# Kernel optimization log

Hardware: AMD Instinct MI355X
Metric: run time of the kernel (lower is better)

## Reference

```python
import jax, jax.numpy as jnp
import numpy as np


def setup_inputs() -> dict:
    key = jax.random.key(0)
    k1, k2 = jax.random.split(key)
    H, W, C = 1024, 2048, 32
    img = jax.random.normal(k1, (1, C, H, W), dtype=jnp.float32)
    flow = jax.random.normal(k2, (1, 2, H, W), dtype=jnp.float32)
    return {"img": img, "flow": flow, "H": H, "W": W}


def reference(img, flow, H, W):
    # img: [1, C, H, W], flow: [1, 2, H, W]
    C = img.shape[1]
    u = flow[:, 0, :, :]  # [1, H, W]
    v = flow[:, 1, :, :]
    grid_x = jnp.arange(W, dtype=jnp.float32)[None, None, :]  # [1,1,W]
    grid_y = jnp.arange(H, dtype=jnp.float32)[None, :, None]  # [1,H,1]
    x = grid_x + u  # [1, H, W]
    y = grid_y + v
    # normalize to [-1, 1] then back (faithful to original two-step mapping)
    x = 2.0 * (x / (W - 1) - 0.5)
    y = 2.0 * (y / (H - 1) - 0.5)
    x = (x + 1.0) * 0.5 * (W - 1)
    y = (y + 1.0) * 0.5 * (H - 1)

    x0 = jnp.floor(x)
    x1 = x0 + 1.0
    y0 = jnp.floor(y)
    y1 = y0 + 1.0
    x0c = jnp.clip(x0, 0, W - 1).astype(jnp.int32)
    x1c = jnp.clip(x1, 0, W - 1).astype(jnp.int32)
    y0c = jnp.clip(y0, 0, H - 1).astype(jnp.int32)
    y1c = jnp.clip(y1, 0, H - 1).astype(jnp.int32)

    # bilinear weights from UNCLAMPED coords (as in the original)
    wa = (x1 - x) * (y1 - y)
    wb = (x1 - x) * (y - y0)
    wc = (x - x0) * (y1 - y)
    wd = (x - x0) * (y - y0)

    img_flat = jnp.transpose(img[0], (1, 2, 0)).reshape(H * W, C)  # [H*W, C]

    def gather_pixel(ix, iy):
        idx = (iy * W + ix).reshape(-1)  # [H*W]
        return jnp.take(img_flat, idx, axis=0)  # [H*W, C]

    Ia = gather_pixel(x0c, y0c)
    Ib = gather_pixel(x0c, y1c)
    Ic = gather_pixel(x1c, y0c)
    Id = gather_pixel(x1c, y1c)

    out = (Ia * wa.reshape(-1, 1) + Ib * wb.reshape(-1, 1)
           + Ic * wc.reshape(-1, 1) + Id * wd.reshape(-1, 1))  # [H*W, C]
    out = out.reshape(1, H, W, C)
    return jnp.transpose(out, (0, 3, 1, 2))  # [1, C, H, W]
```

## Files before the change

kernel.cpp:

```cpp
#include <hip/hip_runtime.h>


#define TSX 64
#define TSY 32
#define RAD 4
#define LW  (TSX + 2*RAD)
#define LH  (TSY + 2*RAD)
#define GPR (LW/4)
#define PLANE (LW*LH)
#define NV  (LH*GPR)
#define CGB 2
#define NSTG (CGB*NV)
#define NTHREADS 1024
#define SOFF (NSTG - NTHREADS)

static_assert(NSTG >= NTHREADS && NSTG <= 2*NTHREADS, "2 slots per thread");

#define GLOAD_LDS16(g, l)                                                  \
    __builtin_amdgcn_global_load_lds(                                      \
        (const __attribute__((address_space(1))) void*)(g),                \
        (__attribute__((address_space(3))) void*)(l), 16, 0, 0)

__global__ __launch_bounds__(NTHREADS, 8) void warp_pipe3(
    const float* __restrict__ img,
    const float* __restrict__ flow,
    const int* __restrict__ Hp,
    const int* __restrict__ Wp,
    float* __restrict__ out,
    int HW, int C)
{
    __shared__ __align__(16) float lds[2 * CGB * PLANE];

    const int W = *Wp;
    const int H = *Hp;
    const int tilesX = (W + TSX - 1) / TSX;
    const int tilesY = (H + TSY - 1) / TSY;
    const int ntiles = tilesX * tilesY;
    const int bid = blockIdx.x;
    if (bid >= ntiles) return;

    const int q = ntiles >> 3, r = ntiles & 7;
    const int xcd = bid & 7, sub = bid >> 3;
    const int t = (xcd < r ? xcd*(q+1) : r*(q+1) + (xcd-r)*q) + sub;

    const int tileY = t / tilesX;
    const int tileX = t - tileY * tilesX;
    const int gx0 = tileX * TSX - RAD;
    const int gy0 = tileY * TSY - RAD;

    const int tid = threadIdx.x;
    const int lx  = tid & 63;
    const int rw  = (tid >> 6) * 2;
    const int gx  = tileX * TSX + lx;

    const float Wm1 = (float)(W - 1);
    const float Hm1 = (float)(H - 1);

    float wtl[2], wth[2], wbl[2], wbh[2];
    int enc[2], pixk[2] = {0, 0};
    #pragma unroll
    for (int k = 0; k < 2; ++k) {
        const int gy = tileY * TSY + rw + k;
        enc[k] = -2;
        if (gx >= W || gy >= H) continue;
        const int pix = gy * W + gx;
        pixk[k] = pix;
        const float u = flow[pix];
        const float v = flow[HW + pix];

        const float x = (float)gx + u;
        const float y = (float)gy + v;
        const float x0 = floorf(x), x1 = x0 + 1.0f;
        const float y0 = floorf(y), y1 = y0 + 1.0f;

        const int x0c = (int)fminf(fmaxf(x0, 0.0f), Wm1);
        const int x1c = (int)fminf(fmaxf(x1, 0.0f), Wm1);
        const int y0c = (int)fminf(fmaxf(y0, 0.0f), Hm1);
        const int y1c = (int)fminf(fmaxf(y1, 0.0f), Hm1);

        const float wa = (x1 - x) * (y1 - y);
        const float wb = (x1 - x) * (y - y0);
        const float wc = (x - x0) * (y1 - y);
        const float wd = (x - x0) * (y - y0);

        const int pbx = min(x0c, W - 2);
        const int pby = min(y0c, H - 2);

        const float wlt = (x0c == pbx ? wa : 0.f) + (x1c == pbx ? wc : 0.f);
        const float wht = (x0c != pbx ? wa : 0.f) + (x1c != pbx ? wc : 0.f);
        const float wlb = (x0c == pbx ? wb : 0.f) + (x1c == pbx ? wd : 0.f);
        const float whb = (x0c != pbx ? wb : 0.f) + (x1c != pbx ? wd : 0.f);
        const bool t0 = (y0c == pby), t1 = (y1c == pby);
        wtl[k] = (t0 ? wlt : 0.f) + (t1 ? wlb : 0.f);
        wth[k] = (t0 ? wht : 0.f) + (t1 ? whb : 0.f);
        wbl[k] = (t0 ? 0.f : wlt) + (t1 ? 0.f : wlb);
        wbh[k] = (t0 ? 0.f : wht) + (t1 ? 0.f : whb);

        const int lxp = pbx - gx0;
        const int lyb = pby - gy0;
        enc[k] = (lxp >= 0 && lxp <= LW-2 && lyb >= 0 && lyb <= LH-2)
               ? (lyb * LW + lxp) : -1;
    }

    float* optr0 = out + pixk[0];
    float* optr1 = out + pixk[1];

    int spix[2], chrel[2], dst4[2];
    #pragma unroll
    for (int s = 0; s < 2; ++s) {
        const int idx = tid + s * SOFF;
        const int ch  = idx / NV;
        const int rem = idx - ch * NV;
        const int rr  = rem / GPR;
        const int g   = rem - rr * GPR;
        const int yy  = min(max(gy0 + rr, 0), H - 1);
        const int xs  = min(max(gx0 + 4*g, 0), W - 4);
        chrel[s] = ch;
        spix[s]  = yy * W + xs;
        dst4[s]  = idx * 4;
    }

    const int nph = (C + CGB - 1) / CGB;
    const bool fast = ((W & 3) == 0) && ((tileX+1)*TSX <= W)
                   && ((tileY+1)*TSY <= H);

    auto gather2 = [&](const float* cur, int c0) {
        #pragma unroll
        for (int k = 0; k < 2; ++k) {
            const int e = enc[k];
            if (e == -2) continue;
            float* o = (k == 0) ? optr0 : optr1;
            if (__builtin_expect(e >= 0, 1)) {
                const float* b0 = cur + e;
                const float a0 = wtl[k], a1 = wth[k];
                const float a2 = wbl[k], a3 = wbh[k];
                o[0] = a0*b0[0] + a1*b0[1] + a2*b0[LW] + a3*b0[LW+1];
                if (c0 + 1 < C)
                    o[HW] = a0*b0[PLANE]   + a1*b0[PLANE+1]
                          + a2*b0[PLANE+LW] + a3*b0[PLANE+LW+1];
            } else {
                const int pix = pixk[k];
                const int gy  = tileY * TSY + rw + k;
                const float u = flow[pix];
                const float v = flow[HW + pix];
                const float x = (float)gx + u;
                const float y = (float)gy + v;
                const float x0 = floorf(x), y0f = floorf(y);
                const int x0c = (int)fminf(fmaxf(x0, 0.f), Wm1);
                const int x1c = (int)fminf(fmaxf(x0 + 1.f, 0.f), Wm1);
                const int y0c = (int)fminf(fmaxf(y0f, 0.f), Hm1);
                const int y1c = (int)fminf(fmaxf(y0f + 1.f, 0.f), Hm1);
                const float wa = (x0 + 1.f - x) * (y0f + 1.f - y);
                const float wb = (x0 + 1.f - x) * (y - y0f);
                const float wc = (x - x0) * (y0f + 1.f - y);
                const float wd = (x - x0) * (y - y0f);
                for (int c = 0; c < CGB && c0 + c < C; ++c) {
                    const float* ic = img + (size_t)(c0 + c) * HW;
                    o[(size_t)c * HW] =
                          wa * ic[(size_t)y0c*W + x0c] + wb * ic[(size_t)y1c*W + x0c]
                        + wc * ic[(size_t)y0c*W + x1c] + wd * ic[(size_t)y1c*W + x1c];
                }
            }
        }
    };

    if (fast) {
        #pragma unroll
        for (int s = 0; s < 2; ++s) {
            const int chc = min(chrel[s], C - 1);
            GLOAD_LDS16(img + (size_t)chc * HW + spix[s], &lds[dst4[s]]);
        }
        asm volatile("s_waitcnt vmcnt(0)" ::: "memory");
        __builtin_amdgcn_s_barrier();
        __builtin_amdgcn_sched_barrier(0);

        float* cur = &lds[0];
        float* nxt = &lds[CGB * PLANE];

        for (int p = 0; p < nph; ++p) {
            const int c0 = p * CGB;

            if (p + 1 < nph) {
                const int c0n = c0 + CGB;
                #pragma unroll
                for (int s = 0; s < 2; ++s) {
                    const int chc = min(c0n + chrel[s], C - 1);
                    GLOAD_LDS16(img + (size_t)chc * HW + spix[s], nxt + dst4[s]);
                }
            }
            __builtin_amdgcn_sched_barrier(0);

            gather2(cur, c0);

            __builtin_amdgcn_sched_barrier(0);

            if (p + 1 < nph) {
                asm volatile("s_waitcnt vmcnt(4)" ::: "memory");
                __builtin_amdgcn_sched_barrier(0);
                __builtin_amdgcn_s_barrier();
                __builtin_amdgcn_sched_barrier(0);
            }
            float* tmp = cur; cur = nxt; nxt = tmp;
            optr0 += (size_t)CGB * HW;
            optr1 += (size_t)CGB * HW;
        }
    } else {
        for (int p = 0; p < nph; ++p) {
            const int c0 = p * CGB;
            __syncthreads();
            for (int i = tid; i < CGB * PLANE; i += NTHREADS) {
                const int ch  = i / PLANE;
                const int rem = i - ch * PLANE;
                const int rr  = rem / LW;
                const int cc  = rem - rr * LW;
                const int yy  = min(max(gy0 + rr, 0), H - 1);
                const int xx  = min(max(gx0 + cc, 0), W - 1);
                const int chc = min(c0 + ch, C - 1);
                lds[i] = img[(size_t)chc * HW + (size_t)yy * W + xx];
            }
            __syncthreads();
            gather2(&lds[0], c0);
            optr0 += (size_t)CGB * HW;
            optr1 += (size_t)CGB * HW;
        }
    }
}

extern "C" void kernel_launch(void* const* d_in, const int* in_sizes, int n_in,
                              void* d_out, int out_size, void* d_ws, size_t ws_size,
                              hipStream_t stream) {
    const float* img  = (const float*)d_in[0];
    const float* flow = (const float*)d_in[1];
    const int*   Hp   = (const int*)d_in[2];
    const int*   Wp   = (const int*)d_in[3];
    float* out = (float*)d_out;

    const int HW = in_sizes[1] / 2;
    const int C  = in_sizes[0] / HW;

    const int grid = (HW + TSX * TSY - 1) / (TSX * TSY) + 64;
    warp_pipe3<<<grid, NTHREADS, 0, stream>>>(img, flow, Hp, Wp, out, HW, C);
}
```

Baseline: 128.4 us.

## Split block into producer/consumer waves with triple-buffered per-channel LDS staging

Replaces the uniform double-buffered two-channel loop with warp specialization. Half the threads (512) compute bilinear weights for 4 pixels each and gather one channel per phase. The other half issue global-to-LDS async loads two channels ahead into a rotating triple buffer. The goal is to keep loads always in flight, decoupled from the gather work. The cost is one barrier per channel instead of per two channels, fewer threads doing the gather math, and more registers per consumer.

New measurement: 212.1 us. 1.65x slower.

```diff
diff --git a/kernel.cpp b/kernel.cpp
--- a/kernel.cpp
+++ b/kernel.cpp
@@ -9,19 +9,17 @@
 #define GPR (LW/4)
 #define PLANE (LW*LH)
 #define NV  (LH*GPR)
-#define CGB 2
-#define NSTG (CGB*NV)
+#define BUFP 4096
 #define NTHREADS 1024
-#define SOFF (NSTG - NTHREADS)
-
-static_assert(NSTG >= NTHREADS && NSTG <= 2*NTHREADS, "2 slots per thread");
+#define NCONS 512
+#define PXT 4
 
 #define GLOAD_LDS16(g, l)                                                  \
     __builtin_amdgcn_global_load_lds(                                      \
         (const __attribute__((address_space(1))) void*)(g),                \
         (__attribute__((address_space(3))) void*)(l), 16, 0, 0)
 
-__global__ __launch_bounds__(NTHREADS, 8) void warp_pipe3(
+__global__ __launch_bounds__(NTHREADS, 8) void warp_pc(
     const float* __restrict__ img,
     const float* __restrict__ flow,
     const int* __restrict__ Hp,
@@ -29,7 +27,7 @@
     float* __restrict__ out,
     int HW, int C)
 {
-    __shared__ __align__(16) float lds[2 * CGB * PLANE];
+    __shared__ __align__(16) float lds[3 * BUFP];
 
     const int W = *Wp;
     const int H = *Hp;
@@ -49,100 +47,104 @@
     const int gy0 = tileY * TSY - RAD;
 
     const int tid = threadIdx.x;
-    const int lx  = tid & 63;
-    const int rw  = (tid >> 6) * 2;
-    const int gx  = tileX * TSX + lx;
+    const bool consumer = (tid < NCONS);
 
     const float Wm1 = (float)(W - 1);
     const float Hm1 = (float)(H - 1);
 
-    float wtl[2], wth[2], wbl[2], wbh[2];
-    int enc[2], pixk[2] = {0, 0};
-    #pragma unroll
-    for (int k = 0; k < 2; ++k) {
-        const int gy = tileY * TSY + rw + k;
-        enc[k] = -2;
-        if (gx >= W || gy >= H) continue;
-        const int pix = gy * W + gx;
-        pixk[k] = pix;
-        const float u = flow[pix];
-        const float v = flow[HW + pix];
-
-        const float x = (float)gx + u;
-        const float y = (float)gy + v;
-        const float x0 = floorf(x), x1 = x0 + 1.0f;
-        const float y0 = floorf(y), y1 = y0 + 1.0f;
-
-        const int x0c = (int)fminf(fmaxf(x0, 0.0f), Wm1);
-        const int x1c = (int)fminf(fmaxf(x1, 0.0f), Wm1);
-        const int y0c = (int)fminf(fmaxf(y0, 0.0f), Hm1);
-        const int y1c = (int)fminf(fmaxf(y1, 0.0f), Hm1);
-
-        const float wa = (x1 - x) * (y1 - y);
-        const float wb = (x1 - x) * (y - y0);
-        const float wc = (x - x0) * (y1 - y);
-        const float wd = (x - x0) * (y - y0);
-
-        const int pbx = min(x0c, W - 2);
-        const int pby = min(y0c, H - 2);
-
-        const float wlt = (x0c == pbx ? wa : 0.f) + (x1c == pbx ? wc : 0.f);
-        const float wht = (x0c != pbx ? wa : 0.f) + (x1c != pbx ? wc : 0.f);
-        const float wlb = (x0c == pbx ? wb : 0.f) + (x1c == pbx ? wd : 0.f);
-        const float whb = (x0c != pbx ? wb : 0.f) + (x1c != pbx ? wd : 0.f);
-        const bool t0 = (y0c == pby), t1 = (y1c == pby);
-        wtl[k] = (t0 ? wlt : 0.f) + (t1 ? wlb : 0.f);
-        wth[k] = (t0 ? wht : 0.f) + (t1 ? whb : 0.f);
-        wbl[k] = (t0 ? 0.f : wlt) + (t1 ? 0.f : wlb);
-        wbh[k] = (t0 ? 0.f : wht) + (t1 ? 0.f : whb);
-
-        const int lxp = pbx - gx0;
-        const int lyb = pby - gy0;
-        enc[k] = (lxp >= 0 && lxp <= LW-2 && lyb >= 0 && lyb <= LH-2)
-               ? (lyb * LW + lxp) : -1;
-    }
-
-    float* optr0 = out + pixk[0];
-    float* optr1 = out + pixk[1];
-
-    int spix[2], chrel[2], dst4[2];
-    #pragma unroll
-    for (int s = 0; s < 2; ++s) {
-        const int idx = tid + s * SOFF;
-        const int ch  = idx / NV;
-        const int rem = idx - ch * NV;
-        const int rr  = rem / GPR;
-        const int g   = rem - rr * GPR;
-        const int yy  = min(max(gy0 + rr, 0), H - 1);
-        const int xs  = min(max(gx0 + 4*g, 0), W - 4);
-        chrel[s] = ch;
-        spix[s]  = yy * W + xs;
-        dst4[s]  = idx * 4;
-    }
-
-    const int nph = (C + CGB - 1) / CGB;
     const bool fast = ((W & 3) == 0) && ((tileX+1)*TSX <= W)
                    && ((tileY+1)*TSY <= H);
 
-    auto gather2 = [&](const float* cur, int c0) {
+    float a0[PXT], a1[PXT], a2[PXT], a3[PXT];
+    int   enc[PXT];
+    float* optr[PXT];
+    int   pixk[PXT];
+    if (consumer) {
         #pragma unroll
-        for (int k = 0; k < 2; ++k) {
-            const int e = enc[k];
+        for (int j = 0; j < PXT; ++j) {
+            const int lpx = j * NCONS + tid;
+            const int col = lpx & (TSX - 1);
+            const int row = lpx >> 6;
+            const int gx = tileX * TSX + col;
+            const int gy = tileY * TSY + row;
+            enc[j] = -2;
+            optr[j] = out; pixk[j] = 0;
+            a0[j] = a1[j] = a2[j] = a3[j] = 0.f;
+            if (gx >= W || gy >= H) continue;
+            const int pix = gy * W + gx;
+            pixk[j] = pix;
+            optr[j] = out + pix;
+            const float u = flow[pix];
+            const float v = flow[HW + pix];
+
+            const float x = (float)gx + u;
+            const float y = (float)gy + v;
+            const float x0 = floorf(x), x1 = x0 + 1.0f;
+            const float y0 = floorf(y), y1 = y0 + 1.0f;
+
+            const int x0c = (int)fminf(fmaxf(x0, 0.0f), Wm1);
+            const int x1c = (int)fminf(fmaxf(x1, 0.0f), Wm1);
+            const int y0c = (int)fminf(fmaxf(y0, 0.0f), Hm1);
+            const int y1c = (int)fminf(fmaxf(y1, 0.0f), Hm1);
+
+            const float wa = (x1 - x) * (y1 - y);
+            const float wb = (x1 - x) * (y - y0);
+            const float wc = (x - x0) * (y1 - y);
+            const float wd = (x - x0) * (y - y0);
+
+            const int pbx = min(x0c, W - 2);
+            const int pby = min(y0c, H - 2);
+
+            const float wlt = (x0c == pbx ? wa : 0.f) + (x1c == pbx ? wc : 0.f);
+            const float wht = (x0c != pbx ? wa : 0.f) + (x1c != pbx ? wc : 0.f);
+            const float wlb = (x0c == pbx ? wb : 0.f) + (x1c == pbx ? wd : 0.f);
+            const float whb = (x0c != pbx ? wb : 0.f) + (x1c != pbx ? wd : 0.f);
+            const bool t0 = (y0c == pby), t1 = (y1c == pby);
+            a0[j] = (t0 ? wlt : 0.f) + (t1 ? wlb : 0.f);
+            a1[j] = (t0 ? wht : 0.f) + (t1 ? whb : 0.f);
+            a2[j] = (t0 ? 0.f : wlt) + (t1 ? 0.f : wlb);
+            a3[j] = (t0 ? 0.f : wht) + (t1 ? 0.f : whb);
+
+            const int lxp = pbx - gx0;
+            const int lyb = pby - gy0;
+            enc[j] = (lxp >= 0 && lxp <= LW-2 && lyb >= 0 && lyb <= LH-2)
+                   ? (lyb * LW + lxp) : -1;
+        }
+    }
+
+    int spix[2] = {0, 0}, dst4[2] = {0, 0};
+    if (!consumer) {
+        const int ptid = tid - NCONS;
+        #pragma unroll
+        for (int s = 0; s < 2; ++s) {
+            const int idx  = ptid + s * NCONS;
+            const int idxe = min(idx, NV - 1);
+            const int rr   = idxe / GPR;
+            const int g    = idxe - rr * GPR;
+            const int yy   = min(max(gy0 + rr, 0), H - 1);
+            const int xs   = min(max(gx0 + 4*g, 0), W - 4);
+            spix[s] = yy * W + xs;
+            dst4[s] = idx * 4;
+        }
+    }
+
+    const int nph = C;
+
+    auto gather = [&](const float* buf, int c) {
+        #pragma unroll
+        for (int j = 0; j < PXT; ++j) {
+            const int e = enc[j];
             if (e == -2) continue;
-            float* o = (k == 0) ? optr0 : optr1;
             if (__builtin_expect(e >= 0, 1)) {
-                const float* b0 = cur + e;
-                const float a0 = wtl[k], a1 = wth[k];
-                const float a2 = wbl[k], a3 = wbh[k];
-                o[0] = a0*b0[0] + a1*b0[1] + a2*b0[LW] + a3*b0[LW+1];
-                if (c0 + 1 < C)
-                    o[HW] = a0*b0[PLANE]   + a1*b0[PLANE+1]
-                          + a2*b0[PLANE+LW] + a3*b0[PLANE+LW+1];
+                const float* b0 = buf + e;
+                *optr[j] = a0[j]*b0[0]  + a1[j]*b0[1]
+                         + a2[j]*b0[LW] + a3[j]*b0[LW+1];
             } else {
-                const int pix = pixk[k];
-                const int gy  = tileY * TSY + rw + k;
+                const int pix = pixk[j];
                 const float u = flow[pix];
                 const float v = flow[HW + pix];
+                const int gx = pix % W;
+                const int gy = pix / W;
                 const float x = (float)gx + u;
                 const float y = (float)gy + v;
                 const float x0 = floorf(x), y0f = floorf(y);
@@ -154,74 +156,65 @@
                 const float wb = (x0 + 1.f - x) * (y - y0f);
                 const float wc = (x - x0) * (y0f + 1.f - y);
                 const float wd = (x - x0) * (y - y0f);
-                for (int c = 0; c < CGB && c0 + c < C; ++c) {
-                    const float* ic = img + (size_t)(c0 + c) * HW;
-                    o[(size_t)c * HW] =
-                          wa * ic[(size_t)y0c*W + x0c] + wb * ic[(size_t)y1c*W + x0c]
-                        + wc * ic[(size_t)y0c*W + x1c] + wd * ic[(size_t)y1c*W + x1c];
-                }
+                const float* ic = img + (size_t)c * HW;
+                *optr[j] = wa * ic[(size_t)y0c*W + x0c]
+                         + wb * ic[(size_t)y1c*W + x0c]
+                         + wc * ic[(size_t)y0c*W + x1c]
+                         + wd * ic[(size_t)y1c*W + x1c];
             }
+            optr[j] += HW;
         }
     };
 
     if (fast) {
-        #pragma unroll
-        for (int s = 0; s < 2; ++s) {
-            const int chc = min(chrel[s], C - 1);
-            GLOAD_LDS16(img + (size_t)chc * HW + spix[s], &lds[dst4[s]]);
-        }
-        asm volatile("s_waitcnt vmcnt(0)" ::: "memory");
+        float* bufA = &lds[0];
+        float* bufB = &lds[BUFP];
+        float* bufC = &lds[2*BUFP];
+
+        if (!consumer) {
+            const size_t c0off = 0;
+            const size_t c1off = (size_t)min(1, C-1) * HW;
+            #pragma unroll
+            for (int s = 0; s < 2; ++s)
+                GLOAD_LDS16(img + c0off + spix[s], bufA + dst4[s]);
+            #pragma unroll
+            for (int s = 0; s < 2; ++s)
+                GLOAD_LDS16(img + c1off + spix[s], bufB + dst4[s]);
+            __builtin_amdgcn_sched_barrier(0);
+            asm volatile("s_waitcnt vmcnt(2)" ::: "memory");
+            __builtin_amdgcn_sched_barrier(0);
+        }
         __builtin_amdgcn_s_barrier();
         __builtin_amdgcn_sched_barrier(0);
 
-        float* cur = &lds[0];
-        float* nxt = &lds[CGB * PLANE];
-
         for (int p = 0; p < nph; ++p) {
-            const int c0 = p * CGB;
-
-            if (p + 1 < nph) {
-                const int c0n = c0 + CGB;
+            if (consumer) {
+                gather(bufA, p);
+            } else {
+                const size_t coff = (size_t)min(p + 2, C - 1) * HW;
                 #pragma unroll
-                for (int s = 0; s < 2; ++s) {
-                    const int chc = min(c0n + chrel[s], C - 1);
-                    GLOAD_LDS16(img + (size_t)chc * HW + spix[s], nxt + dst4[s]);
-                }
-            }
-            __builtin_amdgcn_sched_barrier(0);
-
-            gather2(cur, c0);
-
-            __builtin_amdgcn_sched_barrier(0);
-
-            if (p + 1 < nph) {
-                asm volatile("s_waitcnt vmcnt(4)" ::: "memory");
+                for (int s = 0; s < 2; ++s)
+                    GLOAD_LDS16(img + coff + spix[s], bufC + dst4[s]);
                 __builtin_amdgcn_sched_barrier(0);
-                __builtin_amdgcn_s_barrier();
+                asm volatile("s_waitcnt vmcnt(2)" ::: "memory");
                 __builtin_amdgcn_sched_barrier(0);
             }
-            float* tmp = cur; cur = nxt; nxt = tmp;
-            optr0 += (size_t)CGB * HW;
-            optr1 += (size_t)CGB * HW;
+            __builtin_amdgcn_s_barrier();
+            __builtin_amdgcn_sched_barrier(0);
+            float* tmp = bufA; bufA = bufB; bufB = bufC; bufC = tmp;
         }
     } else {
         for (int p = 0; p < nph; ++p) {
-            const int c0 = p * CGB;
             __syncthreads();
-            for (int i = tid; i < CGB * PLANE; i += NTHREADS) {
-                const int ch  = i / PLANE;
-                const int rem = i - ch * PLANE;
-                const int rr  = rem / LW;
-                const int cc  = rem - rr * LW;
-                const int yy  = min(max(gy0 + rr, 0), H - 1);
-                const int xx  = min(max(gx0 + cc, 0), W - 1);
-                const int chc = min(c0 + ch, C - 1);
-                lds[i] = img[(size_t)chc * HW + (size_t)yy * W + xx];
+            for (int i = tid; i < PLANE; i += NTHREADS) {
+                const int rr = i / LW;
+                const int cc = i - rr * LW;
+                const int yy = min(max(gy0 + rr, 0), H - 1);
+                const int xx = min(max(gx0 + cc, 0), W - 1);
+                lds[i] = img[(size_t)p * HW + (size_t)yy * W + xx];
             }
             __syncthreads();
-            gather2(&lds[0], c0);
-            optr0 += (size_t)CGB * HW;
-            optr1 += (size_t)CGB * HW;
+            if (consumer) gather(&lds[0], p);
         }
     }
 }
@@ -239,5 +232,5 @@
     const int C  = in_sizes[0] / HW;
 
     const int grid = (HW + TSX * TSY - 1) / (TSX * TSY) + 64;
-    warp_pipe3<<<grid, NTHREADS, 0, stream>>>(img, flow, Hp, Wp, out, HW, C);
+    warp_pc<<<grid, NTHREADS, 0, stream>>>(img, flow, Hp, Wp, out, HW, C);
 }
```
